# Kernel optimization log

Measured on AMD Instinct MI355X. Metric: run time of the kernel, lower is better.

## Reference

```python
import jax, jax.numpy as jnp
import numpy as np

GRID_SIZE = 8
MARGIN = 1.0
EPS = 1e-8


def _centers_xy(hc, wc, gs):
    # pixel coordinates of cell centers for a hc x wc grid with stride gs, (x, y) order
    ys = jnp.arange(hc, dtype=jnp.float32) * gs + gs / 2.0 - 0.5
    xs = jnp.arange(wc, dtype=jnp.float32) * gs + gs / 2.0 - 0.5
    gy, gx = jnp.meshgrid(ys, xs, indexing='ij')
    return jnp.stack([gx, gy], axis=-1).reshape(-1, 2)  # (hc*wc, 2)


def _warp_xy(coords_xy, homo):
    # coords_xy: (n,2), homo: (b,3,3) -> (b,n,2) perspective warp
    p = jnp.concatenate([coords_xy, jnp.ones_like(coords_xy[..., :1])], axis=-1)  # (n,3)
    q = jnp.einsum('bij,nj->bni', homo, p)
    return q[..., :2] / (q[..., 2:3] + EPS)


def _bilinear(img, coords_yx):
    # img: (b,c,h,w); coords_yx: (b,n,2) pixel coords -> (b,n,c), zero padding outside
    b, c, h, w = img.shape
    y, x = coords_yx[..., 0], coords_yx[..., 1]
    y0, x0 = jnp.floor(y), jnp.floor(x)
    wy1, wx1 = y - y0, x - x0

    def gat(yi, xi):
        valid = (yi >= 0) & (yi <= h - 1) & (xi >= 0) & (xi <= w - 1)
        yc = jnp.clip(yi, 0, h - 1).astype(jnp.int32)
        xc = jnp.clip(xi, 0, w - 1).astype(jnp.int32)
        v = jax.vmap(lambda im, yy, xx: im[:, yy, xx].T)(img, yc, xc)  # (b,n,c)
        return v * valid[..., None].astype(img.dtype)

    return (gat(y0, x0) * ((1 - wy1) * (1 - wx1))[..., None]
            + gat(y0, x0 + 1) * ((1 - wy1) * wx1)[..., None]
            + gat(y0 + 1, x0) * (wy1 * (1 - wx1))[..., None]
            + gat(y0 + 1, x0 + 1) * (wy1 * wx1)[..., None])


def setup_inputs():
    key = jax.random.key(0)
    k = jax.random.split(key, 6)
    b, c, H, W = 2, 64, 480, 640
    hc, wc = H // GRID_SIZE, W // GRID_SIZE
    score1 = jax.random.uniform(k[0], (b, 1, H, W), dtype=jnp.float32)
    score2 = jax.random.uniform(k[1], (b, 1, H, W), dtype=jnp.float32)
    desc1 = jax.random.normal(k[2], (b, c, hc, wc), dtype=jnp.float32)
    desc1 = desc1 / jnp.linalg.norm(desc1, axis=1, keepdims=True)
    desc2 = jax.random.normal(k[3], (b, c, hc, wc), dtype=jnp.float32)
    desc2 = desc2 / jnp.linalg.norm(desc2, axis=1, keepdims=True)
    homo12 = jnp.eye(3, dtype=jnp.float32)[None] + 0.005 * jax.random.normal(k[4], (b, 3, 3), dtype=jnp.float32)
    homo21 = jnp.linalg.inv(homo12)
    return {"score1": score1, "score2": score2, "desc1": desc1, "desc2": desc2,
            "homo12": homo12, "homo21": homo21}


def reference(score1, score2, desc1, desc2, homo12, homo21):
    b, c, hc, wc = desc1.shape
    H, W = score1.shape[-2], score1.shape[-1]
    n = hc * wc
    gs = GRID_SIZE

    # warp image1 cell centers into image2 pixel space
    coo1_xy = _centers_xy(hc, wc, gs)                 # (n,2) x,y
    w_xy = _warp_xy(coo1_xy, homo12)                  # (b,n,2)
    w_yx = w_xy[..., ::-1]                            # (b,n,2) y,x

    # sample image2 descriptors at warped locations (desc-grid coordinates)
    d_yx = (w_yx - gs / 2.0 + 0.5) / gs
    w_desc1 = _bilinear(desc2, d_yx)                  # (b,n,c)
    w_desc1 = w_desc1 / (jnp.linalg.norm(w_desc1, axis=-1, keepdims=True) + EPS)

    # visibility: warp a ones image by homo21; keep only fully visible cells
    pix_xy = _centers_xy(H, W, 1)                     # (H*W,2)
    wp_xy = _warp_xy(pix_xy, homo21)                  # (b,HW,2)
    ones = jnp.ones((b, 1, H, W), desc1.dtype)
    vis = (_bilinear(ones, wp_xy[..., ::-1]) > 0).astype(desc1.dtype)  # (b,HW,1)
    vis = vis.reshape(b, 1, hc, gs, wc, gs).transpose(0, 3, 5, 1, 2, 4).reshape(b, gs * gs, hc, wc)
    w_vis_mask = jnp.prod(vis, axis=1).reshape(b, 1, n)

    # pairwise coordinate distances + 4-NN neighbor mask
    coo2_yx = _centers_xy(hc, wc, gs)[:, ::-1]        # (n,2) y,x
    a2 = jnp.sum(w_yx * w_yx, axis=-1)                # (b,n)
    b2 = jnp.sum(coo2_yx * coo2_yx, axis=-1)          # (n,)
    coo_dist = jnp.sqrt(jnp.clip(
        a2[:, :, None] + b2[None, None, :] - 2.0 * jnp.einsum('bnd,md->bnm', w_yx, coo2_yx), 0.0))
    _, ids = jax.lax.top_k(-coo_dist, 4)              # 4 smallest distances
    bi = jnp.arange(b)[:, None, None]
    ri = jnp.arange(n)[None, :, None]
    neigh_mask = jnp.zeros_like(coo_dist).at[bi, ri, ids].set(1.0)

    # descriptor inverse-similarity (euclidean distance of unit descriptors)
    d1 = desc1.reshape(b, c, n).transpose(0, 2, 1)    # (b,n,c)
    d2 = desc2.reshape(b, c, n).transpose(0, 2, 1)
    desc_sim = jnp.sqrt(jnp.clip(2.0 - 2.0 * jnp.einsum('bnc,bmc->bnm', d1, d2), EPS))
    desc_sim = desc_sim + neigh_mask * 5.0 + (1.0 - w_vis_mask) * 5.0

    # keypoints whose warps land inside image2
    in_b = ((w_yx[..., 0] >= 0) & (w_yx[..., 0] <= H - 1)
            & (w_yx[..., 1] >= 0) & (w_yx[..., 1] <= W - 1))
    match_mask = in_b.astype(desc1.dtype)             # (b,n)

    pos_sim = jnp.sqrt(jnp.clip(2.0 - 2.0 * jnp.sum(d1 * w_desc1, axis=-1), EPS))
    neg_sim = jnp.min(desc_sim, axis=-1)
    loss = jnp.clip(pos_sim - neg_sim + MARGIN, 0.0) ** 2
    return jnp.sum(loss * match_mask) / jnp.sum(match_mask)
```

## Files before the change

kernel.cpp:

```cpp
#include <hip/hip_runtime.h>
#include <math.h>

#define GS 8
#define HC 60
#define WC 80
#define NN 4800
#define CC 64
#define BB 2
#define HIMG 480
#define WIMG 640
#define EPSF 1e-8f
#define NTILES 75
#define TGN 8
#define BIGF 1e30f

typedef __attribute__((ext_vector_type(8))) short short8v;
typedef __attribute__((ext_vector_type(4))) float f32x4;

__device__ __forceinline__ unsigned short f2bf(float f) {
    unsigned u = __float_as_uint(f);
    u += 0x7FFFu + ((u >> 16) & 1u);
    return (unsigned short)(u >> 16);
}

__global__ __launch_bounds__(256) void k_pre(
    const float* __restrict__ desc1, const float* __restrict__ desc2,
    const float* __restrict__ homo12, const float* __restrict__ homo21,
    unsigned short* __restrict__ d1bf, unsigned short* __restrict__ d2bf,
    float* __restrict__ posim, float* __restrict__ matchm,
    float* __restrict__ biasf, int* __restrict__ neighpk,
    unsigned int* __restrict__ negbits)
{
    __shared__ unsigned short tile[CC][65];
    int bid = blockIdx.x;
    int tid = threadIdx.x;

    if (bid < 2 * BB * NTILES) {
        int arr = bid / (BB * NTILES);
        int rem = bid % (BB * NTILES);
        int b = rem / NTILES;
        int t = rem % NTILES;
        int c0 = t * 64;
        const float* in = arr ? desc2 : desc1;
        unsigned short* out = arr ? d2bf : d1bf;
        int w = tid >> 6, l = tid & 63;
        #pragma unroll
        for (int k = 0; k < 16; k++) {
            int ch = k * 4 + w;
            tile[ch][l] = f2bf(in[((size_t)(b * CC + ch)) * NN + c0 + l]);
        }
        __syncthreads();
        #pragma unroll
        for (int k = 0; k < 16; k++) {
            int cell = k * 4 + w;
            out[((size_t)b * NN + c0 + cell) * CC + l] = tile[l][cell];
        }
        return;
    }

    int sub = bid - 2 * BB * NTILES;
    int wv = tid >> 6, lane = tid & 63;
    int idx = sub * 4 + wv;
    int b = idx / NN, r = idx - b * NN;
    int ci = r / WC, cj = r - ci * WC;

    int allv;
    {
        const float* h = homo21 + b * 9;
        int di = lane >> 3, dj = lane & 7;
        float y = (float)(ci * 8 + di);
        float x = (float)(cj * 8 + dj);
        float qx = h[0]*x + h[1]*y + h[2];
        float qy = h[3]*x + h[4]*y + h[5];
        float qw = h[6]*x + h[7]*y + h[8];
        float px = qx / (qw + EPSF);
        float py = qy / (qw + EPSF);
        float y0 = floorf(py), x0 = floorf(px);
        float ty = py - y0,   tx = px - x0;
        float fyv = ((y0 >= 0.0f && y0 <= (float)(HIMG-1)) ? (1.0f-ty) : 0.0f)
                  + ((y0+1.0f >= 0.0f && y0+1.0f <= (float)(HIMG-1)) ? ty : 0.0f);
        float fxv = ((x0 >= 0.0f && x0 <= (float)(WIMG-1)) ? (1.0f-tx) : 0.0f)
                  + ((x0+1.0f >= 0.0f && x0+1.0f <= (float)(WIMG-1)) ? tx : 0.0f);
        int ok = (fyv > 0.0f && fxv > 0.0f) ? 1 : 0;
        allv = __all(ok);
    }

    const float* h = homo12 + b * 9;
    float xx = cj * 8.0f + 3.5f;
    float yy = ci * 8.0f + 3.5f;
    float qx = h[0]*xx + h[1]*yy + h[2];
    float qy = h[3]*xx + h[4]*yy + h[5];
    float qw = h[6]*xx + h[7]*yy + h[8];
    float wx = qx / (qw + EPSF);
    float wy = qy / (qw + EPSF);
    float dy = (wy - 4.0f + 0.5f) / 8.0f;
    float dx = (wx - 4.0f + 0.5f) / 8.0f;

    float y0f = floorf(dy), x0f = floorf(dx);
    float fy = dy - y0f, fx = dx - x0f;
    float y1f = y0f + 1.0f, x1f = x0f + 1.0f;
    bool v0y = (y0f >= 0.0f && y0f <= (float)(HC-1));
    bool v1y = (y1f >= 0.0f && y1f <= (float)(HC-1));
    bool v0x = (x0f >= 0.0f && x0f <= (float)(WC-1));
    bool v1x = (x1f >= 0.0f && x1f <= (float)(WC-1));
    float w00 = (1.0f-fy)*(1.0f-fx); if (!(v0y && v0x)) w00 = 0.0f;
    float w01 = (1.0f-fy)*fx;        if (!(v0y && v1x)) w01 = 0.0f;
    float w10 = fy*(1.0f-fx);        if (!(v1y && v0x)) w10 = 0.0f;
    float w11 = fy*fx;               if (!(v1y && v1x)) w11 = 0.0f;
    int yc0 = (int)fminf(fmaxf(y0f, 0.0f), (float)(HC-1));
    int yc1 = (int)fminf(fmaxf(y1f, 0.0f), (float)(HC-1));
    int xc0 = (int)fminf(fmaxf(x0f, 0.0f), (float)(WC-1));
    int xc1 = (int)fminf(fmaxf(x1f, 0.0f), (float)(WC-1));
    int o00 = yc0*WC + xc0, o01 = yc0*WC + xc1;
    int o10 = yc1*WC + xc0, o11 = yc1*WC + xc1;

    int ch = lane;
    const float* d2b = desc2 + (size_t)b * CC * NN;
    const float* p = d2b + ch * NN;
    float wvl = w00*p[o00] + w01*p[o01] + w10*p[o10] + w11*p[o11];
    float s2 = wvl * wvl;
    float sd = desc1[((size_t)(b * CC + ch)) * NN + r] * wvl;
    #pragma unroll
    for (int off = 1; off < 64; off <<= 1) {
        s2 += __shfl_xor(s2, off);
        sd += __shfl_xor(sd, off);
    }

    if (lane == 0) {
        biasf[idx] = allv ? 16.0f : 8.0f;
        matchm[idx] = (wy >= 0.0f && wy <= (float)(HIMG-1) &&
                       wx >= 0.0f && wx <= (float)(WIMG-1)) ? 1.0f : 0.0f;
        float dot = sd / (sqrtf(s2) + EPSF);
        posim[idx] = sqrtf(fmaxf(2.0f - 2.0f*dot, EPSF));

        int i0 = (int)floorf(dy);
        int j0 = (int)floorf(dx);
        int ilo = i0 - 1; if (ilo < 0) ilo = 0; if (ilo > HC-4) ilo = HC-4;
        int jlo = j0 - 1; if (jlo < 0) jlo = 0; if (jlo > WC-4) jlo = WC-4;
        float bd0=3e38f, bd1=3e38f, bd2=3e38f, bd3=3e38f;
        int   id0=0,     id1=0,     id2=0,     id3=0;
        #pragma unroll
        for (int a = 0; a < 4; a++) {
            float cy = (float)(ilo + a) * 8.0f + 3.5f;
            float ddy = wy - cy;
            float ddy2 = ddy * ddy;
            #pragma unroll
            for (int q = 0; q < 4; q++) {
                float cx = (float)(jlo + q) * 8.0f + 3.5f;
                float ddx = wx - cx;
                float dv = ddy2 + ddx * ddx;
                int id = (ilo + a) * WC + (jlo + q);
                if (dv < bd3) {
                    bd3 = dv; id3 = id;
                    if (bd3 < bd2) { float tf=bd2; bd2=bd3; bd3=tf; int ti=id2; id2=id3; id3=ti; }
                    if (bd2 < bd1) { float tf=bd1; bd1=bd2; bd2=tf; int ti=id1; id1=id2; id2=ti; }
                    if (bd1 < bd0) { float tf=bd0; bd0=bd1; bd1=tf; int ti=id0; id0=id1; id1=ti; }
                }
            }
        }
        int base = ilo * WC + jlo;
        int mask = 0;
        {
            int d, ri, rj;
            d = id0 - base; ri = d / WC; rj = d - ri * WC; mask |= 1 << (ri*4+rj);
            d = id1 - base; ri = d / WC; rj = d - ri * WC; mask |= 1 << (ri*4+rj);
            d = id2 - base; ri = d / WC; rj = d - ri * WC; mask |= 1 << (ri*4+rj);
            d = id3 - base; ri = d / WC; rj = d - ri * WC; mask |= 1 << (ri*4+rj);
        }
        neighpk[idx] = mask | (ilo << 16) | (jlo << 24);
        negbits[idx] = 0x7F800000u;
    }
}


#define GLL(gp, lp) __builtin_amdgcn_global_load_lds(                        \
    (const __attribute__((address_space(1))) unsigned int*)(gp),             \
    (__attribute__((address_space(3))) unsigned int*)(lp), 16, 0, 0)

__global__ __launch_bounds__(256) void k_negmin(
    const unsigned short* __restrict__ d1bf, const unsigned short* __restrict__ d2bf,
    const float* __restrict__ biasf, const int* __restrict__ neighpk,
    unsigned int* __restrict__ negbits)
{
    __shared__ unsigned short Bsm[2][4096];

    int bid = blockIdx.x;
    int b   = bid / (150 * TGN);
    int rem = bid % (150 * TGN);
    int rb  = rem >> 3;
    int tg  = rem & 7;
    int tid = threadIdx.x;
    int w   = tid >> 6;
    int lane = tid & 63;
    int l15 = lane & 15, lg = lane >> 4;
    int r0  = rb * 32;
    int wl  = w * 16 + l15;
    int lg8 = lg * 8;
    int bNN = b * NN;

    const unsigned short* d1b = d1bf + (size_t)bNN * CC;
    const unsigned short* d2b = d2bf + (size_t)bNN * CC;

    short8v afr00 = *(const short8v*)(d1b + (size_t)(r0 + l15) * CC + lg8);
    short8v afr01 = *(const short8v*)(d1b + (size_t)(r0 + l15) * CC + 32 + lg8);
    short8v afr10 = *(const short8v*)(d1b + (size_t)(r0 + 16 + l15) * CC + lg8);
    short8v afr11 = *(const short8v*)(d1b + (size_t)(r0 + 16 + l15) * CC + 32 + lg8);

    int pk[8];
    int lmin = 0x7FFFFFFF, lmax = -1;
    #pragma unroll
    for (int s_ = 0; s_ < 8; s_++) {
        int row = r0 + (s_ >> 2) * 16 + lg * 4 + (s_ & 3);
        int p = neighpk[bNN + row];
        pk[s_] = p;
        int ilo = (p >> 16) & 0xFF, jlo = (p >> 24) & 0xFF;
        int idm = ilo * WC + jlo;
        lmin = min(lmin, idm);
        lmax = max(lmax, idm + 3 * WC + 3);
    }
    #pragma unroll
    for (int off = 1; off < 64; off <<= 1) {
        lmin = min(lmin, __shfl_xor(lmin, off));
        lmax = max(lmax, __shfl_xor(lmax, off));
    }

    float m[8];
    #pragma unroll
    for (int i = 0; i < 8; i++) m[i] = -BIGF;

    int o0 = w * 64 + lane;
    int o1 = o0 + 256;
    int s0 = (o0 & ~7) | ((o0 ^ (o0 >> 3)) & 7);
    int s1 = (o1 & ~7) | ((o1 ^ (o1 >> 3)) & 7);

    int nt = (NTILES - tg + 7) >> 3;

    {
        const unsigned short* tb0 = d2b + (size_t)(tg * 64) * CC;
        GLL(tb0 + s0 * 8, &Bsm[0][w * 512]);
        GLL(tb0 + s1 * 8, &Bsm[0][2048 + w * 512]);
    }
    float bias = biasf[bNN + tg * 64 + wl];
    __syncthreads();

    int buf = 0;
    for (int it = 0; it < nt; it++) {
        int t = tg + it * 8;

        float bias_n = 0.0f;
        if (it + 1 < nt) {
            const unsigned short* tbn = d2b + (size_t)((t + 8) * 64) * CC;
            GLL(tbn + s0 * 8, &Bsm[buf ^ 1][w * 512]);
            GLL(tbn + s1 * 8, &Bsm[buf ^ 1][2048 + w * 512]);
            bias_n = biasf[bNN + (t + 8) * 64 + wl];
        }

        const unsigned short* lb = &Bsm[buf][0];
        short8v b0 = *(const short8v*)(lb + (size_t)wl * 64 + (size_t)((lg ^ wl) & 7) * 8);
        short8v b1 = *(const short8v*)(lb + (size_t)wl * 64 + (size_t)(((4 + lg) ^ wl) & 7) * 8);

        f32x4 a0 = {bias, bias, bias, bias};
        f32x4 a1 = a0;
        a0 = __builtin_amdgcn_mfma_f32_16x16x32_bf16(afr00, b0, a0, 0, 0, 0);
        a0 = __builtin_amdgcn_mfma_f32_16x16x32_bf16(afr01, b1, a0, 0, 0, 0);
        a1 = __builtin_amdgcn_mfma_f32_16x16x32_bf16(afr10, b0, a1, 0, 0, 0);
        a1 = __builtin_amdgcn_mfma_f32_16x16x32_bf16(afr11, b1, a1, 0, 0, 0);

        int tb = t * 64;
        if (tb + 63 < lmin || tb > lmax) {
            #pragma unroll
            for (int g_ = 0; g_ < 4; g_++) {
                m[g_]   = fmaxf(m[g_],   a0[g_]);
                m[4+g_] = fmaxf(m[4+g_], a1[g_]);
            }
        } else {
            int c_ = tb + wl;
            int gi_ = c_ / WC; int gj_ = c_ - gi_ * WC;
            #pragma unroll
            for (int s_ = 0; s_ < 8; s_++) {
                int p_ = pk[s_]; int msk_ = p_ & 0xFFFF;
                unsigned ri_ = (unsigned)(gi_ - ((p_ >> 16) & 0xFF));
                unsigned rj_ = (unsigned)(gj_ - ((p_ >> 24) & 0xFF));
                unsigned bx_ = (ri_ < 4u && rj_ < 4u) ? (ri_ * 4u + rj_) : 16u;
                bool nb_ = ((msk_ >> bx_) & 1) != 0;
                float sv_ = (s_ < 4) ? a0[s_ & 3] : a1[s_ & 3];
                float key_ = nb_ ? sv_ - 8.0f : sv_;
                m[s_] = fmaxf(m[s_], key_);
            }
        }

        bias = bias_n;
        buf ^= 1;
        __syncthreads();
    }

    #pragma unroll
    for (int s_ = 0; s_ < 8; s_++) {
        float mv = m[s_];
        float pen, sdot;
        if (mv >= 12.0f)     { pen = 0.0f;  sdot = mv - 16.0f; }
        else if (mv >= 4.0f) { pen = 5.0f;  sdot = mv - 8.0f; }
        else                 { pen = 10.0f; sdot = mv; }
        float res = sqrtf(fmaxf(2.0f - 2.0f * sdot, EPSF)) + pen;
        #pragma unroll
        for (int off = 1; off < 16; off <<= 1)
            res = fminf(res, __shfl_xor(res, off));
        if (l15 == 0) {
            int row = r0 + (s_ >> 2) * 16 + lg * 4 + (s_ & 3);
            atomicMin(&negbits[bNN + row], __float_as_uint(res));
        }
    }
}

__global__ void k_loss(const float* __restrict__ posim, const float* __restrict__ matchm,
                       const unsigned int* __restrict__ negbits, float* __restrict__ bpart)
{
    __shared__ float sn[256], sdn[256];
    int tid = threadIdx.x;
    int idx = blockIdx.x * 256 + tid;
    float num = 0.0f, den = 0.0f;
    if (idx < BB * NN) {
        float neg = __uint_as_float(negbits[idx]);
        float l = fmaxf(posim[idx] - neg + 1.0f, 0.0f);
        float mm = matchm[idx];
        num = l * l * mm;
        den = mm;
    }
    sn[tid] = num; sdn[tid] = den;
    __syncthreads();
    for (int st = 128; st > 0; st >>= 1) {
        if (tid < st) { sn[tid] += sn[tid + st]; sdn[tid] += sdn[tid + st]; }
        __syncthreads();
    }
    if (tid == 0) { bpart[blockIdx.x * 2] = sn[0]; bpart[blockIdx.x * 2 + 1] = sdn[0]; }
}

__global__ void k_sum(const float* __restrict__ bpart, int nb, float* __restrict__ out)
{
    int t = threadIdx.x;
    float num = 0.0f, den = 0.0f;
    if (t < nb) { num = bpart[t * 2]; den = bpart[t * 2 + 1]; }
    #pragma unroll
    for (int off = 1; off < 64; off <<= 1) {
        num += __shfl_xor(num, off);
        den += __shfl_xor(den, off);
    }
    if (t == 0) out[0] = num / den;
}

extern "C" void kernel_launch(void* const* d_in, const int* in_sizes, int n_in,
                              void* d_out, int out_size, void* d_ws, size_t ws_size,
                              hipStream_t stream)
{
    const float* desc1  = (const float*)d_in[2];
    const float* desc2  = (const float*)d_in[3];
    const float* homo12 = (const float*)d_in[4];
    const float* homo21 = (const float*)d_in[5];
    float* out = (float*)d_out;

    float*        biasf   = (float*)d_ws;
    float*        posim   = biasf + BB * NN;
    float*        matchm  = posim + BB * NN;
    int*          neighpk = (int*)(matchm + BB * NN);
    unsigned int* negbits = (unsigned int*)(neighpk + BB * NN);
    float*        bpart   = (float*)(negbits + BB * NN);
    unsigned short* d1bf  = (unsigned short*)(bpart + 128);
    unsigned short* d2bf  = d1bf + (size_t)BB * NN * CC;

    int nb = (BB * NN + 255) / 256;
    int nb_pre = 2 * BB * NTILES + 2 * BB * NTILES * 4;
    k_pre<<<nb_pre, 256, 0, stream>>>(desc1, desc2, homo12, homo21,
                                      d1bf, d2bf, posim, matchm, biasf, neighpk, negbits);
    k_negmin<<<BB * 150 * TGN, 256, 0, stream>>>(d1bf, d2bf, biasf, neighpk, negbits);
    k_loss<<<nb, 256, 0, stream>>>(posim, matchm, negbits, bpart);
    k_sum<<<1, 64, 0, stream>>>(bpart, nb, out);
}
```

Before: 43.95 us.

## Fuse loss reduction into negmin via last-block pattern and triple-buffer tiles

Measured after the change: 61.55 us. 40.1% more time.

```diff
diff --git a/kernel.cpp b/kernel.cpp
--- a/kernel.cpp
+++ b/kernel.cpp
@@ -11,7 +11,9 @@
 #define WIMG 640
 #define EPSF 1e-8f
 #define NTILES 75
-#define TGN 8
+#define TGN 5
+#define NT 15
+#define NBLK (BB * 150 * TGN)
 #define BIGF 1e30f
 
 typedef __attribute__((ext_vector_type(8))) short short8v;
@@ -29,13 +31,14 @@
     unsigned short* __restrict__ d1bf, unsigned short* __restrict__ d2bf,
     float* __restrict__ posim, float* __restrict__ matchm,
     float* __restrict__ biasf, int* __restrict__ neighpk,
-    unsigned int* __restrict__ negbits)
+    unsigned int* __restrict__ negbits, unsigned int* __restrict__ donecnt)
 {
     __shared__ unsigned short tile[CC][65];
     int bid = blockIdx.x;
     int tid = threadIdx.x;
 
     if (bid < 2 * BB * NTILES) {
+        if (bid == 0 && tid == 0) donecnt[0] = 0u;
         int arr = bid / (BB * NTILES);
         int rem = bid % (BB * NTILES);
         int b = rem / NTILES;
@@ -177,18 +180,24 @@
     (const __attribute__((address_space(1))) unsigned int*)(gp),             \
     (__attribute__((address_space(3))) unsigned int*)(lp), 16, 0, 0)
 
+#define MFMA16(A, B, C) __builtin_amdgcn_mfma_f32_16x16x32_bf16((A), (B), (C), 0, 0, 0)
+
 __global__ __launch_bounds__(256) void k_negmin(
     const unsigned short* __restrict__ d1bf, const unsigned short* __restrict__ d2bf,
     const float* __restrict__ biasf, const int* __restrict__ neighpk,
-    unsigned int* __restrict__ negbits)
+    unsigned int* __restrict__ negbits,
+    const float* __restrict__ posim, const float* __restrict__ matchm,
+    unsigned int* __restrict__ donecnt, float* __restrict__ out)
 {
-    __shared__ unsigned short Bsm[2][4096];
+    __shared__ unsigned short Bsm[3][4096];
+    __shared__ float sn[256], sdn[256];
+    __shared__ int lastflag;
 
     int bid = blockIdx.x;
     int b   = bid / (150 * TGN);
     int rem = bid % (150 * TGN);
-    int rb  = rem >> 3;
-    int tg  = rem & 7;
+    int rb  = rem / TGN;
+    int tg  = rem % TGN;
     int tid = threadIdx.x;
     int w   = tid >> 6;
     int lane = tid & 63;
@@ -224,6 +233,11 @@
         lmax = max(lmax, __shfl_xor(lmax, off));
     }
 
+    float biasv[NT];
+    #pragma unroll
+    for (int i = 0; i < NT; i++)
+        biasv[i] = biasf[bNN + (tg + TGN * i) * 64 + wl];
+
     float m[8];
     #pragma unroll
     for (int i = 0; i < 8; i++) m[i] = -BIGF;
@@ -233,66 +247,64 @@
     int s0 = (o0 & ~7) | ((o0 ^ (o0 >> 3)) & 7);
     int s1 = (o1 & ~7) | ((o1 ^ (o1 >> 3)) & 7);
 
-    int nt = (NTILES - tg + 7) >> 3;
-
-    {
-        const unsigned short* tb0 = d2b + (size_t)(tg * 64) * CC;
-        GLL(tb0 + s0 * 8, &Bsm[0][w * 512]);
-        GLL(tb0 + s1 * 8, &Bsm[0][2048 + w * 512]);
-    }
-    float bias = biasf[bNN + tg * 64 + wl];
-    __syncthreads();
-
-    int buf = 0;
-    for (int it = 0; it < nt; it++) {
-        int t = tg + it * 8;
-
-        float bias_n = 0.0f;
-        if (it + 1 < nt) {
-            const unsigned short* tbn = d2b + (size_t)((t + 8) * 64) * CC;
-            GLL(tbn + s0 * 8, &Bsm[buf ^ 1][w * 512]);
-            GLL(tbn + s1 * 8, &Bsm[buf ^ 1][2048 + w * 512]);
-            bias_n = biasf[bNN + (t + 8) * 64 + wl];
-        }
-
-        const unsigned short* lb = &Bsm[buf][0];
-        short8v b0 = *(const short8v*)(lb + (size_t)wl * 64 + (size_t)((lg ^ wl) & 7) * 8);
-        short8v b1 = *(const short8v*)(lb + (size_t)wl * 64 + (size_t)(((4 + lg) ^ wl) & 7) * 8);
-
-        f32x4 a0 = {bias, bias, bias, bias};
-        f32x4 a1 = a0;
-        a0 = __builtin_amdgcn_mfma_f32_16x16x32_bf16(afr00, b0, a0, 0, 0, 0);
-        a0 = __builtin_amdgcn_mfma_f32_16x16x32_bf16(afr01, b1, a0, 0, 0, 0);
-        a1 = __builtin_amdgcn_mfma_f32_16x16x32_bf16(afr10, b0, a1, 0, 0, 0);
-        a1 = __builtin_amdgcn_mfma_f32_16x16x32_bf16(afr11, b1, a1, 0, 0, 0);
-
-        int tb = t * 64;
-        if (tb + 63 < lmin || tb > lmax) {
-            #pragma unroll
-            for (int g_ = 0; g_ < 4; g_++) {
-                m[g_]   = fmaxf(m[g_],   a0[g_]);
-                m[4+g_] = fmaxf(m[4+g_], a1[g_]);
-            }
-        } else {
-            int c_ = tb + wl;
-            int gi_ = c_ / WC; int gj_ = c_ - gi_ * WC;
-            #pragma unroll
-            for (int s_ = 0; s_ < 8; s_++) {
-                int p_ = pk[s_]; int msk_ = p_ & 0xFFFF;
-                unsigned ri_ = (unsigned)(gi_ - ((p_ >> 16) & 0xFF));
-                unsigned rj_ = (unsigned)(gj_ - ((p_ >> 24) & 0xFF));
-                unsigned bx_ = (ri_ < 4u && rj_ < 4u) ? (ri_ * 4u + rj_) : 16u;
-                bool nb_ = ((msk_ >> bx_) & 1) != 0;
-                float sv_ = (s_ < 4) ? a0[s_ & 3] : a1[s_ & 3];
-                float key_ = nb_ ? sv_ - 8.0f : sv_;
-                m[s_] = fmaxf(m[s_], key_);
-            }
-        }
-
-        bias = bias_n;
-        buf ^= 1;
-        __syncthreads();
-    }
+#define STAGEI(I) do {                                                       \
+    const unsigned short* tbp_ = d2b + (size_t)((tg + TGN * (I)) * 64) * CC; \
+    GLL(tbp_ + s0 * 8, &Bsm[(I) % 3][w * 512]);                              \
+    GLL(tbp_ + s1 * 8, &Bsm[(I) % 3][2048 + w * 512]);                       \
+} while (0)
+
+#define COMPI(I) do {                                                        \
+    const unsigned short* lb_ = &Bsm[(I) % 3][0];                            \
+    short8v b0_ = *(const short8v*)(lb_ + (size_t)wl * 64 +                  \
+                                    (size_t)((lg ^ wl) & 7) * 8);            \
+    short8v b1_ = *(const short8v*)(lb_ + (size_t)wl * 64 +                  \
+                                    (size_t)(((4 + lg) ^ wl) & 7) * 8);      \
+    float bi_ = biasv[I];                                                    \
+    f32x4 a0_ = {bi_, bi_, bi_, bi_};                                        \
+    f32x4 a1_ = a0_;                                                         \
+    a0_ = MFMA16(afr00, b0_, a0_);                                           \
+    a0_ = MFMA16(afr01, b1_, a0_);                                           \
+    a1_ = MFMA16(afr10, b0_, a1_);                                           \
+    a1_ = MFMA16(afr11, b1_, a1_);                                           \
+    int tb_ = (tg + TGN * (I)) * 64;                                         \
+    if (tb_ + 63 < lmin || tb_ > lmax) {                                     \
+        _Pragma("unroll")                                                    \
+        for (int g_ = 0; g_ < 4; g_++) {                                     \
+            m[g_]     = fmaxf(m[g_],     a0_[g_]);                           \
+            m[4 + g_] = fmaxf(m[4 + g_], a1_[g_]);                           \
+        }                                                                    \
+    } else {                                                                 \
+        int c_ = tb_ + wl;                                                   \
+        int gi_ = c_ / WC; int gj_ = c_ - gi_ * WC;                          \
+        _Pragma("unroll")                                                    \
+        for (int s_ = 0; s_ < 8; s_++) {                                     \
+            int p_ = pk[s_]; int msk_ = p_ & 0xFFFF;                         \
+            unsigned ri_ = (unsigned)(gi_ - ((p_ >> 16) & 0xFF));            \
+            unsigned rj_ = (unsigned)(gj_ - ((p_ >> 24) & 0xFF));            \
+            unsigned bx_ = (ri_ < 4u && rj_ < 4u) ? (ri_ * 4u + rj_) : 16u;  \
+            bool nb_ = ((msk_ >> bx_) & 1) != 0;                             \
+            float sv_ = (s_ < 4) ? a0_[s_ & 3] : a1_[s_ & 3];                \
+            float key_ = nb_ ? sv_ - 8.0f : sv_;                             \
+            m[s_] = fmaxf(m[s_], key_);                                      \
+        }                                                                    \
+    }                                                                        \
+} while (0)
+
+#define ITER(I, VMC) do {                                                    \
+    if ((I) + 2 < NT) STAGEI((I) + 2);                                       \
+    asm volatile("s_waitcnt vmcnt(" #VMC ")\n\ts_barrier" ::: "memory");     \
+    COMPI(I);                                                                \
+    asm volatile("s_barrier" ::: "memory");                                  \
+} while (0)
+
+    STAGEI(0);
+    STAGEI(1);
+
+    ITER(0, 4);  ITER(1, 4);  ITER(2, 4);  ITER(3, 4);  ITER(4, 4);
+    ITER(5, 4);  ITER(6, 4);  ITER(7, 4);  ITER(8, 4);  ITER(9, 4);
+    ITER(10, 4); ITER(11, 4); ITER(12, 4);
+    ITER(13, 2);
+    ITER(14, 0);
 
     #pragma unroll
     for (int s_ = 0; s_ < 8; s_++) {
@@ -310,42 +322,33 @@
             atomicMin(&negbits[bNN + row], __float_as_uint(res));
         }
     }
-}
-
-__global__ void k_loss(const float* __restrict__ posim, const float* __restrict__ matchm,
-                       const unsigned int* __restrict__ negbits, float* __restrict__ bpart)
-{
-    __shared__ float sn[256], sdn[256];
-    int tid = threadIdx.x;
-    int idx = blockIdx.x * 256 + tid;
-    float num = 0.0f, den = 0.0f;
-    if (idx < BB * NN) {
-        float neg = __uint_as_float(negbits[idx]);
-        float l = fmaxf(posim[idx] - neg + 1.0f, 0.0f);
-        float mm = matchm[idx];
-        num = l * l * mm;
-        den = mm;
-    }
-    sn[tid] = num; sdn[tid] = den;
+
     __syncthreads();
-    for (int st = 128; st > 0; st >>= 1) {
-        if (tid < st) { sn[tid] += sn[tid + st]; sdn[tid] += sdn[tid + st]; }
+    if (tid == 0) {
+        unsigned old = atomicAdd(donecnt, 1u);
+        lastflag = (old == (unsigned)(NBLK - 1)) ? 1 : 0;
+    }
+    __syncthreads();
+    if (lastflag) {
+        __threadfence();
+        float num = 0.0f, den = 0.0f;
+        for (int i = tid; i < BB * NN; i += 256) {
+            unsigned nbv = __hip_atomic_load(&negbits[i], __ATOMIC_RELAXED,
+                                             __HIP_MEMORY_SCOPE_AGENT);
+            float neg = __uint_as_float(nbv);
+            float l = fmaxf(posim[i] - neg + 1.0f, 0.0f);
+            float mm = matchm[i];
+            num += l * l * mm;
+            den += mm;
+        }
+        sn[tid] = num; sdn[tid] = den;
         __syncthreads();
-    }
-    if (tid == 0) { bpart[blockIdx.x * 2] = sn[0]; bpart[blockIdx.x * 2 + 1] = sdn[0]; }
-}
-
-__global__ void k_sum(const float* __restrict__ bpart, int nb, float* __restrict__ out)
-{
-    int t = threadIdx.x;
-    float num = 0.0f, den = 0.0f;
-    if (t < nb) { num = bpart[t * 2]; den = bpart[t * 2 + 1]; }
-    #pragma unroll
-    for (int off = 1; off < 64; off <<= 1) {
-        num += __shfl_xor(num, off);
-        den += __shfl_xor(den, off);
-    }
-    if (t == 0) out[0] = num / den;
+        for (int s = 128; s > 0; s >>= 1) {
+            if (tid < s) { sn[tid] += sn[tid + s]; sdn[tid] += sdn[tid + s]; }
+            __syncthreads();
+        }
+        if (tid == 0) out[0] = sn[0] / sdn[0];
+    }
 }
 
 extern "C" void kernel_launch(void* const* d_in, const int* in_sizes, int n_in,
@@ -363,15 +366,14 @@
     float*        matchm  = posim + BB * NN;
     int*          neighpk = (int*)(matchm + BB * NN);
     unsigned int* negbits = (unsigned int*)(neighpk + BB * NN);
-    float*        bpart   = (float*)(negbits + BB * NN);
-    unsigned short* d1bf  = (unsigned short*)(bpart + 128);
+    unsigned int* donecnt = negbits + BB * NN;
+    unsigned short* d1bf  = (unsigned short*)(donecnt + 64);
     unsigned short* d2bf  = d1bf + (size_t)BB * NN * CC;
 
-    int nb = (BB * NN + 255) / 256;
     int nb_pre = 2 * BB * NTILES + 2 * BB * NTILES * 4;
     k_pre<<<nb_pre, 256, 0, stream>>>(desc1, desc2, homo12, homo21,
-                                      d1bf, d2bf, posim, matchm, biasf, neighpk, negbits);
-    k_negmin<<<BB * 150 * TGN, 256, 0, stream>>>(d1bf, d2bf, biasf, neighpk, negbits);
-    k_loss<<<nb, 256, 0, stream>>>(posim, matchm, negbits, bpart);
-    k_sum<<<1, 64, 0, stream>>>(bpart, nb, out);
+                                      d1bf, d2bf, posim, matchm, biasf, neighpk,
+                                      negbits, donecnt);
+    k_negmin<<<NBLK, 256, 0, stream>>>(d1bf, d2bf, biasf, neighpk, negbits,
+                                       posim, matchm, donecnt, out);
 }
```
